# Kernel tuning notes

Measured on AMD Instinct MI355X. Metric: run time of the kernel, lower is better.

The kernel has to match this reference:

```python
import jax, jax.numpy as jnp
import numpy as np

NUM_CAPSULE = 32
DIM_VECTOR = 16
NUM_ROUTING = 3

def squash(v, axis=-1):
    s2 = jnp.sum(jnp.square(v), axis=axis, keepdims=True)
    scale = s2 / (1.0 + s2) / jnp.sqrt(s2)
    return scale * v

def setup_inputs() -> dict:
    key = jax.random.key(0)
    k1, k2 = jax.random.split(key)
    B, IN_CAPS, IN_DIM = 64, 2048, 8
    x = jax.random.normal(k1, (B, IN_CAPS, IN_DIM), dtype=jnp.float32)
    # glorot-uniform-ish weight: [in_caps, num_caps, in_dim, out_dim]
    limit = np.sqrt(6.0 / (IN_DIM + DIM_VECTOR)).astype(np.float32)
    W = jax.random.uniform(k2, (IN_CAPS, NUM_CAPSULE, IN_DIM, DIM_VECTOR), dtype=jnp.float32, minval=-limit, maxval=limit)
    return {"x": x, "W": W}

def reference(x, W):
    # x: [B, in_caps, in_dim]; W: [in_caps, num_caps, in_dim, out_dim]
    # inputs_hat (u_hat): [B, in_caps, num_caps, out_dim]
    u_hat = jnp.einsum('bid,inde->bine', x, W)
    B, IN_CAPS = u_hat.shape[0], u_hat.shape[1]
    # routing logits; original broadcasts over out_dim with identical values,
    # so a trailing singleton dim is mathematically equivalent
    b = jnp.zeros((B, IN_CAPS, NUM_CAPSULE, 1), dtype=u_hat.dtype)
    v = None
    for i in range(NUM_ROUTING):
        c = jax.nn.softmax(b, axis=2)                       # over num_capsule
        s = jnp.sum(c * u_hat, axis=1, keepdims=True)       # [B,1,nc,out]
        v = squash(s)                                       # [B,1,nc,out]
        if i != NUM_ROUTING - 1:
            b = b + jnp.sum(u_hat * v, axis=-1, keepdims=True)
    return v.reshape(-1, NUM_CAPSULE, DIM_VECTOR)
```

## Files before the change

kernel.cpp:

```cpp
#include <hip/hip_runtime.h>
#include <math.h>


#define B_TOT 64
#define I_TOT 2048
#define D_IN  8
#define NC    32
#define EV    16
#define OD    (NC*EV)
#define BC    8
#define NBC   (B_TOT/BC)
#define BC0   16
#define NBC0  (B_TOT/BC0)
#define ICH   8
#define NIC   (I_TOT/ICH)
#define S_ELEMS (B_TOT*OD)

__device__ __forceinline__ void fma4(float4& acc, float a, const float4& w) {
    acc.x = fmaf(a, w.x, acc.x);
    acc.y = fmaf(a, w.y, acc.y);
    acc.z = fmaf(a, w.z, acc.z);
    acc.w = fmaf(a, w.w, acc.w);
}

__global__ __launch_bounds__(256, 4)
void route0(const float* __restrict__ x, const float* __restrict__ W,
            float* __restrict__ P)
{
    __shared__ __align__(16) float xl[BC0 * ICH * D_IN];

    const int t  = threadIdx.x;
    const int ic = blockIdx.x & (NIC - 1);
    const int bc = blockIdx.x >> 8;
    const int b0 = bc * BC0;
    const int i0 = ic * ICH;
    const int eq = t & 3;
    const int bh = (t >> 2) & 1;
    const int n  = t >> 3;

    {
        const int row = t >> 4, f = (t & 15) * 4;
        *(float4*)&xl[row * (ICH * D_IN) + f] =
            *(const float4*)&x[((size_t)(b0 + row) * I_TOT + i0) * D_IN + f];
    }
    __syncthreads();

    float4 sacc[8];
    #pragma unroll
    for (int q = 0; q < 8; ++q) sacc[q] = make_float4(0.f, 0.f, 0.f, 0.f);

    const float* Wt = &W[(size_t)i0 * 4096 + n * 128 + eq * 4];

    #pragma unroll 1
    for (int ii = 0; ii < ICH; ++ii) {
        const int iir = (ii + bc * 2) & 7;
        float4 wr[8];
        #pragma unroll
        for (int d = 0; d < 8; ++d)
            wr[d] = *(const float4*)&Wt[iir * 4096 + d * 16];

        #pragma unroll
        for (int q = 0; q < 8; ++q) {
            const int bl = bh * 8 + q;
            float4 xa = *(float4*)&xl[bl * (ICH * D_IN) + iir * 8];
            float4 xb = *(float4*)&xl[bl * (ICH * D_IN) + iir * 8 + 4];
            fma4(sacc[q], xa.x, wr[0]); fma4(sacc[q], xa.y, wr[1]);
            fma4(sacc[q], xa.z, wr[2]); fma4(sacc[q], xa.w, wr[3]);
            fma4(sacc[q], xb.x, wr[4]); fma4(sacc[q], xb.y, wr[5]);
            fma4(sacc[q], xb.z, wr[6]); fma4(sacc[q], xb.w, wr[7]);
        }
    }

    #pragma unroll
    for (int q = 0; q < 8; ++q)
        *(float4*)&P[((size_t)ic * B_TOT + b0 + bh * 8 + q) * OD + n * EV + eq * 4] = sacc[q];
}

__global__ __launch_bounds__(256, 4)
void route1(const float* __restrict__ x, const float* __restrict__ W,
            float* __restrict__ P, const float* __restrict__ vin)
{
    __shared__ __align__(16) float xl[BC * ICH * D_IN];
    __shared__ float wsum[2][4][BC];

    const int t  = threadIdx.x;
    const int ic = blockIdx.x & (NIC - 1);
    const int bc = blockIdx.x >> 8;
    const int b0 = bc * BC;
    const int i0 = ic * ICH;
    const int eq = t & 3;
    const int bh = (t >> 2) & 1;
    const int n  = t >> 3;
    const int w  = t >> 6;

    if (t < 128) {
        const int row = t >> 4, f = (t & 15) * 4;
        *(float4*)&xl[row * (ICH * D_IN) + f] =
            *(const float4*)&x[((size_t)(b0 + row) * I_TOT + i0) * D_IN + f];
    }

    float4 vr[4];
    #pragma unroll
    for (int q = 0; q < 4; ++q)
        vr[q] = *(const float4*)&vin[(size_t)(b0 + bh * 4 + q) * OD + n * EV + eq * 4];
    __syncthreads();

    float4 sacc[4];
    #pragma unroll
    for (int q = 0; q < 4; ++q) sacc[q] = make_float4(0.f, 0.f, 0.f, 0.f);

    const float* Wt = &W[(size_t)i0 * 4096 + n * 128 + eq * 4];

    #pragma unroll 1
    for (int ii = 0; ii < ICH; ++ii) {
        const int iir = (ii + bc) & 7;
        float4 wr[8];
        #pragma unroll
        for (int d = 0; d < 8; ++d)
            wr[d] = *(const float4*)&Wt[iir * 4096 + d * 16];

        float4 u[4];
        #pragma unroll
        for (int q = 0; q < 4; ++q) {
            const int bl = bh * 4 + q;
            float4 xa = *(float4*)&xl[bl * (ICH * D_IN) + iir * 8];
            float4 xb = *(float4*)&xl[bl * (ICH * D_IN) + iir * 8 + 4];
            float4 uu = make_float4(0.f, 0.f, 0.f, 0.f);
            fma4(uu, xa.x, wr[0]); fma4(uu, xa.y, wr[1]);
            fma4(uu, xa.z, wr[2]); fma4(uu, xa.w, wr[3]);
            fma4(uu, xb.x, wr[4]); fma4(uu, xb.y, wr[5]);
            fma4(uu, xb.z, wr[6]); fma4(uu, xb.w, wr[7]);
            u[q] = uu;
        }

        float a[4];
        #pragma unroll
        for (int q = 0; q < 4; ++q) {
            float ap = u[q].x * vr[q].x + u[q].y * vr[q].y
                     + u[q].z * vr[q].z + u[q].w * vr[q].w;
            ap += __shfl_xor(ap, 1, 64);
            ap += __shfl_xor(ap, 2, 64);
            a[q] = ap;
        }
        float e[4], p[4];
        #pragma unroll
        for (int q = 0; q < 4; ++q) {
            e[q] = __expf(a[q]);
            float pp = e[q];
            pp += __shfl_xor(pp, 8, 64);
            pp += __shfl_xor(pp, 16, 64);
            pp += __shfl_xor(pp, 32, 64);
            p[q] = pp;
        }
        if (eq == 0) {
            #pragma unroll
            for (int q = 0; q < 4; ++q)
                wsum[ii & 1][w][bh * 4 + q] = p[q];
        }
        __syncthreads();
        #pragma unroll
        for (int q = 0; q < 4; ++q) {
            const int bl = bh * 4 + q;
            float s = wsum[ii & 1][0][bl] + wsum[ii & 1][1][bl]
                    + wsum[ii & 1][2][bl] + wsum[ii & 1][3][bl];
            float c = e[q] / s;
            fma4(sacc[q], c, u[q]);
        }
    }

    #pragma unroll
    for (int q = 0; q < 4; ++q)
        *(float4*)&P[((size_t)ic * B_TOT + b0 + bh * 4 + q) * OD + n * EV + eq * 4] = sacc[q];
}

__global__ __launch_bounds__(256, 4)
void reduce_sq(const float* __restrict__ P, float* __restrict__ dst,
               const float* __restrict__ addsrc, float pre)
{
    __shared__ float red[256];
    const int b   = blockIdx.x >> 3;
    const int oq  = blockIdx.x & 7;
    const int t   = threadIdx.x;
    const int o   = oq * 64 + (t & 63);
    const int icq = t >> 6;
    const size_t stride = (size_t)B_TOT * OD;

    float acc = 0.f;
    size_t base = ((size_t)(icq * 64) * B_TOT + b) * OD + o;
    #pragma unroll 8
    for (int k = 0; k < 64; ++k) acc += P[base + (size_t)k * stride];
    red[t] = acc;
    __syncthreads();

    if (t < 64) {
        float v = (red[t] + red[t + 64] + red[t + 128] + red[t + 192]) * pre;
        float q2 = v * v;
        q2 += __shfl_xor(q2, 1, 64);
        q2 += __shfl_xor(q2, 2, 64);
        q2 += __shfl_xor(q2, 4, 64);
        q2 += __shfl_xor(q2, 8, 64);
        float sc = q2 / ((1.0f + q2) * sqrtf(q2));
        float outv = v * sc;
        if (addsrc) outv += addsrc[(size_t)b * OD + o];
        dst[(size_t)b * OD + o] = outv;
    }
}

extern "C" void kernel_launch(void* const* d_in, const int* in_sizes, int n_in,
                              void* d_out, int out_size, void* d_ws, size_t ws_size,
                              hipStream_t stream) {
    const float* x = (const float*)d_in[0];
    const float* W = (const float*)d_in[1];
    float* out = (float*)d_out;

    char* ws = (char*)d_ws;
    float* P  = (float*)ws;
    float* v0 = (float*)(ws + (size_t)32 * 1024 * 1024);
    float* vs = v0 + S_ELEMS;

    dim3 r0g(NBC0 * NIC), r1g(NBC * NIC), rb(256);
    dim3 sg(B_TOT * 8), sb(256);

    route0<<<r0g, rb, 0, stream>>>(x, W, P);
    reduce_sq<<<sg, sb, 0, stream>>>(P, v0, nullptr, 1.0f / 32.0f);
    route1<<<r1g, rb, 0, stream>>>(x, W, P, v0);
    reduce_sq<<<sg, sb, 0, stream>>>(P, vs, v0, 1.0f);
    route1<<<r1g, rb, 0, stream>>>(x, W, P, vs);
    reduce_sq<<<sg, sb, 0, stream>>>(P, out, nullptr, 1.0f);
}
```

Baseline: 191.4 us.

## Fuse first routing pass with reduction and squash into a single kernel

Replaces the initial partial-sum kernel plus separate reduce/squash pass with one kernel where each block handles one output capsule and 8 batches over all input capsules. The block reduces across 16 input-capsule slices in shared memory and applies squash directly. This removes the partial buffer write/read and one launch, but rereads W once per 8-batch chunk and rereads x once per output capsule, increasing global load traffic.

```diff
diff --git a/kernel.cpp b/kernel.cpp
--- a/kernel.cpp
+++ b/kernel.cpp
@@ -10,8 +10,6 @@
 #define OD    (NC*EV)
 #define BC    8
 #define NBC   (B_TOT/BC)
-#define BC0   16
-#define NBC0  (B_TOT/BC0)
 #define ICH   8
 #define NIC   (I_TOT/ICH)
 #define S_ELEMS (B_TOT*OD)
@@ -23,57 +21,59 @@
     acc.w = fmaf(a, w.w, acc.w);
 }
 
-__global__ __launch_bounds__(256, 4)
-void route0(const float* __restrict__ x, const float* __restrict__ W,
-            float* __restrict__ P)
+__global__ __launch_bounds__(512)
+void route0d(const float* __restrict__ x, const float* __restrict__ W,
+             float* __restrict__ v0)
 {
-    __shared__ __align__(16) float xl[BC0 * ICH * D_IN];
+    __shared__ __align__(16) float4 red[512];
 
     const int t  = threadIdx.x;
-    const int ic = blockIdx.x & (NIC - 1);
-    const int bc = blockIdx.x >> 8;
-    const int b0 = bc * BC0;
-    const int i0 = ic * ICH;
+    const int n  = blockIdx.x & 31;
+    const int bc = blockIdx.x >> 5;
+    const int b0 = bc * 8;
     const int eq = t & 3;
-    const int bh = (t >> 2) & 1;
-    const int n  = t >> 3;
-
-    {
-        const int row = t >> 4, f = (t & 15) * 4;
-        *(float4*)&xl[row * (ICH * D_IN) + f] =
-            *(const float4*)&x[((size_t)(b0 + row) * I_TOT + i0) * D_IN + f];
-    }
+    const int b  = (t >> 2) & 7;
+    const int ks = t >> 5;
+
+    const float* Wn = W + n * 128 + eq * 4;
+    const float* xb = x + (size_t)(b0 + b) * I_TOT * D_IN;
+
+    float4 acc = make_float4(0.f, 0.f, 0.f, 0.f);
+    const int iA = ks * 128;
+
+    #pragma unroll 1
+    for (int io = 0; io < 128; ++io) {
+        const size_t i = (size_t)(iA + io);
+        float4 wr[8];
+        #pragma unroll
+        for (int d = 0; d < 8; ++d)
+            wr[d] = *(const float4*)&Wn[i * 4096 + d * 16];
+        float4 xa = *(const float4*)&xb[i * 8];
+        float4 xc = *(const float4*)&xb[i * 8 + 4];
+        fma4(acc, xa.x, wr[0]); fma4(acc, xa.y, wr[1]);
+        fma4(acc, xa.z, wr[2]); fma4(acc, xa.w, wr[3]);
+        fma4(acc, xc.x, wr[4]); fma4(acc, xc.y, wr[5]);
+        fma4(acc, xc.z, wr[6]); fma4(acc, xc.w, wr[7]);
+    }
+    red[t] = acc;
     __syncthreads();
 
-    float4 sacc[8];
-    #pragma unroll
-    for (int q = 0; q < 8; ++q) sacc[q] = make_float4(0.f, 0.f, 0.f, 0.f);
-
-    const float* Wt = &W[(size_t)i0 * 4096 + n * 128 + eq * 4];
-
-    #pragma unroll 1
-    for (int ii = 0; ii < ICH; ++ii) {
-        const int iir = (ii + bc * 2) & 7;
-        float4 wr[8];
-        #pragma unroll
-        for (int d = 0; d < 8; ++d)
-            wr[d] = *(const float4*)&Wt[iir * 4096 + d * 16];
-
-        #pragma unroll
-        for (int q = 0; q < 8; ++q) {
-            const int bl = bh * 8 + q;
-            float4 xa = *(float4*)&xl[bl * (ICH * D_IN) + iir * 8];
-            float4 xb = *(float4*)&xl[bl * (ICH * D_IN) + iir * 8 + 4];
-            fma4(sacc[q], xa.x, wr[0]); fma4(sacc[q], xa.y, wr[1]);
-            fma4(sacc[q], xa.z, wr[2]); fma4(sacc[q], xa.w, wr[3]);
-            fma4(sacc[q], xb.x, wr[4]); fma4(sacc[q], xb.y, wr[5]);
-            fma4(sacc[q], xb.z, wr[6]); fma4(sacc[q], xb.w, wr[7]);
-        }
-    }
-
-    #pragma unroll
-    for (int q = 0; q < 8; ++q)
-        *(float4*)&P[((size_t)ic * B_TOT + b0 + bh * 8 + q) * OD + n * EV + eq * 4] = sacc[q];
+    if (t < 32) {
+        float4 s = red[t];
+        #pragma unroll
+        for (int j = 1; j < 16; ++j) {
+            float4 r = red[t + j * 32];
+            s.x += r.x; s.y += r.y; s.z += r.z; s.w += r.w;
+        }
+        const float pre = 1.0f / 32.0f;
+        s.x *= pre; s.y *= pre; s.z *= pre; s.w *= pre;
+        float q2 = s.x*s.x + s.y*s.y + s.z*s.z + s.w*s.w;
+        q2 += __shfl_xor(q2, 1, 64);
+        q2 += __shfl_xor(q2, 2, 64);
+        float sc = q2 / ((1.0f + q2) * sqrtf(q2));
+        s.x *= sc; s.y *= sc; s.z *= sc; s.w *= sc;
+        *(float4*)&v0[(size_t)(b0 + b) * OD + n * EV + eq * 4] = s;
+    }
 }
 
 __global__ __launch_bounds__(256, 4)
@@ -218,11 +218,11 @@
     float* v0 = (float*)(ws + (size_t)32 * 1024 * 1024);
     float* vs = v0 + S_ELEMS;
 
-    dim3 r0g(NBC0 * NIC), r1g(NBC * NIC), rb(256);
+    dim3 g0(NBC * NC), b0k(512);
+    dim3 r1g(NBC * NIC), rb(256);
     dim3 sg(B_TOT * 8), sb(256);
 
-    route0<<<r0g, rb, 0, stream>>>(x, W, P);
-    reduce_sq<<<sg, sb, 0, stream>>>(P, v0, nullptr, 1.0f / 32.0f);
+    route0d<<<g0, b0k, 0, stream>>>(x, W, v0);
     route1<<<r1g, rb, 0, stream>>>(x, W, P, v0);
     reduce_sq<<<sg, sb, 0, stream>>>(P, vs, v0, 1.0f);
     route1<<<r1g, rb, 0, stream>>>(x, W, P, vs);
```

Result: slower. 229.1 us (+19.7%).
